# Optimization experiments

Measured on AMD Instinct MI355X. Metric: run time of the kernel, lower is better.

The kernel has to match this reference:

```python
import jax, jax.numpy as jnp
import numpy as np

N = 262144   # active voxels
C = 128      # channels (in == out)
B, Z, Y, X = 2, 41, 512, 512
EPS = 1e-3   # BN eps from norm_cfg


def _build_neighbors():
    """Build submanifold rulebook-style neighbor tables along z, y, x axes.
    Each table is [N, 3] (offsets -1, 0, +1); missing neighbor -> sentinel N
    (points at a zero-padded feature row)."""
    rng = np.random.default_rng(0)
    total = B * Z * Y * X
    lin = np.sort(rng.choice(total, size=N, replace=False)).astype(np.int64)
    lookup = np.full(total, -1, dtype=np.int64)
    lookup[lin] = np.arange(N)
    r = lin % (Z * Y * X)
    z = r // (Y * X)
    r2 = r % (Y * X)
    y = r2 // X
    x = r2 % X

    def nbrs(axis_vals, axis_size, stride):
        cols = []
        for off in (-1, 0, 1):
            v = axis_vals + off
            valid = (v >= 0) & (v < axis_size)
            nlin = np.clip(lin + off * stride, 0, total - 1)
            idx = np.where(valid, lookup[nlin], -1)
            idx = np.where(idx < 0, N, idx)
            cols.append(idx)
        return np.stack(cols, axis=1).astype(np.int32)

    return nbrs(z, Z, Y * X), nbrs(y, Y, X), nbrs(x, X, 1)


def setup_inputs() -> dict:
    key = jax.random.key(0)
    ks = jax.random.split(key, 8)
    nbr_z, nbr_y, nbr_x = _build_neighbors()
    scale = 1.0 / np.sqrt(3 * C)
    inp = {
        "features": jax.random.normal(ks[0], (N, C), dtype=jnp.float32),
        "W1": jax.random.normal(ks[1], (3, C, C), dtype=jnp.float32) * scale,  # conv3x1x1
        "W2": jax.random.normal(ks[2], (3, C, C), dtype=jnp.float32) * scale,  # conv1x3x1
        "W3": jax.random.normal(ks[3], (3, C, C), dtype=jnp.float32) * scale,  # conv1x1x3
        "g0": jax.random.normal(ks[4], (C,), dtype=jnp.float32) * 0.1 + 1.0,
        "b0": jnp.zeros((C,), dtype=jnp.float32),
        "m0": jax.random.normal(ks[5], (C,), dtype=jnp.float32) * 0.1,
        "v0": jax.random.uniform(ks[5], (C,), minval=0.5, maxval=1.5, dtype=jnp.float32),
        "g2": jax.random.normal(ks[6], (C,), dtype=jnp.float32) * 0.1 + 1.0,
        "b2": jnp.zeros((C,), dtype=jnp.float32),
        "m2": jax.random.normal(ks[6], (C,), dtype=jnp.float32) * 0.1,
        "v2": jax.random.uniform(ks[6], (C,), minval=0.5, maxval=1.5, dtype=jnp.float32),
        "g3": jax.random.normal(ks[7], (C,), dtype=jnp.float32) * 0.1 + 1.0,
        "b3": jnp.zeros((C,), dtype=jnp.float32),
        "m3": jax.random.normal(ks[7], (C,), dtype=jnp.float32) * 0.1,
        "v3": jax.random.uniform(ks[7], (C,), minval=0.5, maxval=1.5, dtype=jnp.float32),
        "nbr_z": jnp.asarray(nbr_z),
        "nbr_y": jnp.asarray(nbr_y),
        "nbr_x": jnp.asarray(nbr_x),
    }
    return inp


def _subm_conv(feats, nbr, W):
    # submanifold gather-matmul: out[n] = sum_k W[k] @ feats[nbr[n,k]] (sentinel -> 0)
    feats_pad = jnp.concatenate([feats, jnp.zeros((1, feats.shape[1]), feats.dtype)], axis=0)
    gathered = feats_pad[nbr]  # [N, 3, C]
    return jnp.einsum('nkc,kcd->nd', gathered, W)


def _bn(x, g, b, m, v):
    return (x - m) * (g * jax.lax.rsqrt(v + EPS)) + b


def reference(features, W1, W2, W3, g0, b0, m0, v0, g2, b2, m2, v2,
              g3, b3, m3, v3, nbr_z, nbr_y, nbr_x):
    # Branch 1: conv3x1x1 -> bn0 -> sigmoid, then (source bug) bn0_2 -> sigmoid applied again
    s = jax.nn.sigmoid(_bn(_subm_conv(features, nbr_z, W1), g0, b0, m0, v0))
    s = jax.nn.sigmoid(_bn(s, g2, b2, m2, v2))
    # Branch 2: conv1x3x1, added raw (its BN/act were mistakenly applied to branch 1)
    s2 = _subm_conv(features, nbr_y, W2)
    # Branch 3: conv1x1x3 -> bn0_3 -> sigmoid
    s3 = jax.nn.sigmoid(_bn(_subm_conv(features, nbr_x, W3), g3, b3, m3, v3))
    return (s + s2 + s3) * features
```

## Files before the change

### kernel.cpp

```cpp
#include <hip/hip_runtime.h>
#include <hip/hip_bf16.h>
#include <stdint.h>
#include <stddef.h>

#define NVOX 262144
#define CCH 128
#define BN_EPS 1e-3f

typedef __attribute__((ext_vector_type(8))) short bfrag;
typedef __attribute__((ext_vector_type(4))) float f4;

#define AS1 __attribute__((address_space(1)))
#define AS3 __attribute__((address_space(3)))

__device__ __forceinline__ unsigned short f2bf(float f) {
  union { float f; unsigned u; } v; v.f = f;
  unsigned r = v.u + 0x7fffu + ((v.u >> 16) & 1u);
  return (unsigned short)(r >> 16);
}

__device__ __forceinline__ bfrag pack8(f4 x, f4 y) {
  bfrag r;
  r[0] = (short)f2bf(x[0]); r[1] = (short)f2bf(x[1]);
  r[2] = (short)f2bf(x[2]); r[3] = (short)f2bf(x[3]);
  r[4] = (short)f2bf(y[0]); r[5] = (short)f2bf(y[1]);
  r[6] = (short)f2bf(y[2]); r[7] = (short)f2bf(y[3]);
  return r;
}

__device__ __forceinline__ float sigmoidf_(float x) {
  const float e = __builtin_amdgcn_exp2f(x * -1.44269504f);
  return __builtin_amdgcn_rcpf(1.f + e);
}

__device__ __forceinline__ float bf2f(unsigned short h) {
  union { unsigned u; float f; } v; v.u = ((unsigned)h) << 16; return v.f;
}

__global__ void prep_wfrag(const float* __restrict__ W1, const float* __restrict__ W2,
                           const float* __restrict__ W3, unsigned short* __restrict__ wf) {
  const int frag = blockIdx.x;
  const int tile = frag & 7;
  const int kc   = (frag >> 3) & 3;
  const int tap  = (frag >> 5) % 3;
  const int conv = frag / 96;
  const float* W = (conv == 0) ? W1 : ((conv == 1) ? W2 : W3);
  const int l   = threadIdx.x;
  const int col = tile * 16 + (l & 15);
  const int k0  = kc * 32 + (l >> 4) * 8;
  bfrag o;
#pragma unroll
  for (int e = 0; e < 8; ++e)
    o[e] = (short)f2bf(W[(size_t)(tap * CCH + k0 + e) * CCH + col]);
  *reinterpret_cast<bfrag*>(wf + (size_t)frag * 512 + l * 8) = o;
}

__global__ void prep_bn(const float* g0, const float* b0, const float* m0, const float* v0,
                        const float* g2, const float* b2, const float* m2, const float* v2,
                        const float* g3, const float* b3, const float* m3, const float* v3,
                        float* __restrict__ bn) {
  const int c = threadIdx.x;
  const float s0 = g0[c] * rsqrtf(v0[c] + BN_EPS);
  const float s2 = g2[c] * rsqrtf(v2[c] + BN_EPS);
  const float s3 = g3[c] * rsqrtf(v3[c] + BN_EPS);
  bn[0 * CCH + c] = s0; bn[1 * CCH + c] = b0[c] - m0[c] * s0;
  bn[2 * CCH + c] = s2; bn[3 * CCH + c] = b2[c] - m2[c] * s2;
  bn[4 * CCH + c] = s3; bn[5 * CCH + c] = b3[c] - m3[c] * s3;
}

__global__ void prep_bf16(const float* __restrict__ feats, unsigned short* __restrict__ fbf) {
  const size_t base = ((size_t)blockIdx.x * 256 + threadIdx.x) * 8;
  const f4 x = *reinterpret_cast<const f4*>(feats + base);
  const f4 y = *reinterpret_cast<const f4*>(feats + base + 4);
  *reinterpret_cast<bfrag*>(fbf + base) = pack8(x, y);
  if (blockIdx.x == 0 && threadIdx.x < 16) {
    bfrag z = {0, 0, 0, 0, 0, 0, 0, 0};
    *reinterpret_cast<bfrag*>(fbf + (size_t)NVOX * CCH + threadIdx.x * 8) = z;
  }
}

__global__ __launch_bounds__(512, 3)
void recon_v20(const unsigned short* __restrict__ fbf,
               const unsigned short* __restrict__ wfrag,
               const float* __restrict__ bn,
               const int* __restrict__ nbrz, const int* __restrict__ nbrx,
               const int* __restrict__ nbry,
               float* __restrict__ out) {
  __shared__ unsigned short Bb[24576];

  const int tid  = threadIdx.x;
  const int lane = tid & 63;
  const int w    = tid >> 6;
  const int l15  = lane & 15;
  const int lhi  = lane >> 4;
  const int cb   = blockIdx.x & 1;
  const int row0 = (blockIdx.x >> 1) * 128;
  const int wrow = row0 + w * 16;

  auto fillconv = [&](int RB) {
#pragma unroll
    for (int i = 0; i < 6; ++i) {
      const int L    = w * 6 + i;
      const int slot = L >> 4;
      const int sub  = L & 15;
      const int g    = ((RB + slot) * 4 + (sub >> 2)) * 8 + cb * 4 + (sub & 3);
      __builtin_amdgcn_global_load_lds(
          (const AS1 void*)(wfrag + (size_t)g * 512 + lane * 8),
          (AS3 void*)((char*)Bb + L * 1024), 16, 0, 0);
    }
  };

  fillconv(0);
  const int row = wrow + l15;
  const int rg  = row * 3;
  const int izp = nbrz[rg + 0], izn = nbrz[rg + 2];
  const int ixp = nbrx[rg + 0], ixn = nbrx[rg + 2];
  const int iyp = nbry[rg + 0], iyn = nbry[rg + 2];

  const bool azp = __any(izp != NVOX), azn = __any(izn != NVOX);
  const bool axp = __any(ixp != NVOX), axn = __any(ixn != NVOX);
  const bool ayp = __any(iyp != NVOX), ayn = __any(iyn != NVOX);

  bfrag aF[4];
  bfrag aS[4];

#define LOADF(DST, IDX) {                                                     \
    const char* p = (const char*)fbf + ((size_t)(unsigned)(IDX) << 8) + (lhi << 4); \
    DST[0] = *reinterpret_cast<const bfrag*>(p);                              \
    DST[1] = *reinterpret_cast<const bfrag*>(p + 64);                         \
    DST[2] = *reinterpret_cast<const bfrag*>(p + 128);                        \
    DST[3] = *reinterpret_cast<const bfrag*>(p + 192);                        \
  }

#define TAP(SLOT, AFR, ACCS) {                                                \
    const char* bs = (const char*)Bb + (SLOT) * 16384 + lane * 16;            \
    _Pragma("unroll")                                                         \
    for (int kc = 0; kc < 4; ++kc) {                                          \
      _Pragma("unroll")                                                       \
      for (int ct = 0; ct < 4; ++ct) {                                        \
        const bfrag b = *reinterpret_cast<const bfrag*>(                      \
            bs + (kc * 4 + ct) * 1024);                                       \
        ACCS[ct] = __builtin_amdgcn_mfma_f32_16x16x32_bf16(                   \
            AFR[kc], b, ACCS[ct], 0, 0, 0);                                   \
      } } }

#define CONVBODY(VP, VN, IN, ACCS)                                            \
  {                                                                           \
    TAP(1, aS, ACCS)                                                          \
    if (VP) {                                                                 \
      TAP(0, aF, ACCS)                                                        \
      if (VN) { LOADF(aF, IN)  TAP(2, aF, ACCS) }                             \
    } else if (VN) {                                                          \
      TAP(2, aF, ACCS)                                                        \
    }                                                                         \
  }

  LOADF(aS, row)
  if (azp)      LOADF(aF, izp)
  else if (azn) LOADF(aF, izn)

  __syncthreads();

  f4 acc[4], run[4];
#pragma unroll
  for (int ct = 0; ct < 4; ++ct) {
    acc[ct] = f4{0.f, 0.f, 0.f, 0.f};
    run[ct] = f4{0.f, 0.f, 0.f, 0.f};
  }

  CONVBODY(azp, azn, izn, acc)
  __syncthreads();
  fillconv(6);
  if (axp)      LOADF(aF, ixp)
  else if (axn) LOADF(aF, ixn)
#pragma unroll
  for (int ct = 0; ct < 4; ++ct) {
    const int col = cb * 64 + ct * 16 + l15;
    const float sc0 = bn[0 * CCH + col], sh0 = bn[1 * CCH + col];
    const float sc2 = bn[2 * CCH + col], sh2 = bn[3 * CCH + col];
#pragma unroll
    for (int j = 0; j < 4; ++j) {
      const float u = sigmoidf_(sc0 * acc[ct][j] + sh0);
      run[ct][j] = sigmoidf_(sc2 * u + sh2);
    }
    acc[ct] = f4{0.f, 0.f, 0.f, 0.f};
  }
  __syncthreads();

  CONVBODY(axp, axn, ixn, acc)
  __syncthreads();
  fillconv(3);
  if (ayp)      LOADF(aF, iyp)
  else if (ayn) LOADF(aF, iyn)
#pragma unroll
  for (int ct = 0; ct < 4; ++ct) {
    const int col = cb * 64 + ct * 16 + l15;
    const float sc3 = bn[4 * CCH + col], sh3 = bn[5 * CCH + col];
#pragma unroll
    for (int j = 0; j < 4; ++j)
      run[ct][j] += sigmoidf_(sc3 * acc[ct][j] + sh3);
  }
  __syncthreads();

  CONVBODY(ayp, ayn, iyn, run)

#undef CONVBODY
#undef TAP
#undef LOADF

#pragma unroll
  for (int ct = 0; ct < 4; ++ct) {
    const int col = cb * 64 + ct * 16 + l15;
#pragma unroll
    for (int j = 0; j < 4; ++j) {
      const int r = wrow + (lhi << 2) + j;
      const size_t o = ((size_t)r << 7) + col;
      out[o] = run[ct][j] * bf2f(fbf[o]);
    }
  }
}

__global__ void recon_naive(const float* __restrict__ feats,
    const float* __restrict__ W1, const float* __restrict__ W2, const float* __restrict__ W3,
    const int* __restrict__ nbrz, const int* __restrict__ nbry, const int* __restrict__ nbrx,
    const float* g0, const float* b0, const float* m0, const float* v0,
    const float* g2, const float* b2, const float* m2, const float* v2,
    const float* g3, const float* b3, const float* m3, const float* v3,
    float* __restrict__ out) {
  __shared__ float rows[3][CCH];
  const int n = blockIdx.x;
  const int d = threadIdx.x;
  float res[3];
#pragma unroll
  for (int conv = 0; conv < 3; ++conv) {
    const int* nbr  = (conv == 0) ? nbrz : ((conv == 1) ? nbry : nbrx);
    const float* W  = (conv == 0) ? W1 : ((conv == 1) ? W2 : W3);
#pragma unroll
    for (int tap = 0; tap < 3; ++tap) {
      const int idx = nbr[n * 3 + tap];
      rows[tap][d] = ((unsigned)idx < (unsigned)NVOX) ? feats[((size_t)idx << 7) + d] : 0.f;
    }
    __syncthreads();
    const float* rflat = &rows[0][0];
    float s = 0.f;
    for (int k = 0; k < 3 * CCH; ++k) s += rflat[k] * W[(size_t)k * CCH + d];
    res[conv] = s;
    __syncthreads();
  }
  const float sc0 = g0[d] * rsqrtf(v0[d] + BN_EPS), sh0 = b0[d] - m0[d] * sc0;
  const float sc2 = g2[d] * rsqrtf(v2[d] + BN_EPS), sh2 = b2[d] - m2[d] * sc2;
  const float sc3 = g3[d] * rsqrtf(v3[d] + BN_EPS), sh3 = b3[d] - m3[d] * sc3;
  float u = 1.f / (1.f + __expf(-(sc0 * res[0] + sh0)));
  u = 1.f / (1.f + __expf(-(sc2 * u + sh2)));
  const float s3v = 1.f / (1.f + __expf(-(sc3 * res[2] + sh3)));
  out[((size_t)n << 7) + d] = (u + res[1] + s3v) * feats[((size_t)n << 7) + d];
}

extern "C" void kernel_launch(void* const* d_in, const int* in_sizes, int n_in,
                              void* d_out, int out_size, void* d_ws, size_t ws_size,
                              hipStream_t stream) {
  const float* feats = (const float*)d_in[0];
  const float* W1 = (const float*)d_in[1];
  const float* W2 = (const float*)d_in[2];
  const float* W3 = (const float*)d_in[3];
  const float* g0 = (const float*)d_in[4];
  const float* b0 = (const float*)d_in[5];
  const float* m0 = (const float*)d_in[6];
  const float* v0 = (const float*)d_in[7];
  const float* g2 = (const float*)d_in[8];
  const float* b2 = (const float*)d_in[9];
  const float* m2 = (const float*)d_in[10];
  const float* v2 = (const float*)d_in[11];
  const float* g3 = (const float*)d_in[12];
  const float* b3 = (const float*)d_in[13];
  const float* m3 = (const float*)d_in[14];
  const float* v3 = (const float*)d_in[15];
  const int* nz = (const int*)d_in[16];
  const int* ny = (const int*)d_in[17];
  const int* nx = (const int*)d_in[18];
  float* out = (float*)d_out;

  const size_t wf_bytes = 288u * 1024u;
  const size_t bn_bytes = 4096u;
  const size_t fb_bytes = ((size_t)NVOX + 1) * CCH * sizeof(short);
  if (ws_size >= wf_bytes + bn_bytes + fb_bytes) {
    unsigned short* wf  = (unsigned short*)d_ws;
    float*          bnt = (float*)((char*)d_ws + wf_bytes);
    unsigned short* fbf = (unsigned short*)((char*)d_ws + wf_bytes + bn_bytes);
    hipLaunchKernelGGL(prep_wfrag, dim3(288), dim3(64), 0, stream, W1, W2, W3, wf);
    hipLaunchKernelGGL(prep_bn, dim3(1), dim3(CCH), 0, stream,
                       g0, b0, m0, v0, g2, b2, m2, v2, g3, b3, m3, v3, bnt);
    hipLaunchKernelGGL(prep_bf16, dim3((NVOX * CCH) / (256 * 8)), dim3(256), 0, stream,
                       feats, fbf);
    hipLaunchKernelGGL(recon_v20, dim3((NVOX / 128) * 2), dim3(512), 0, stream,
                       fbf, wf, bnt, nz, nx, ny, out);
  } else {
    hipLaunchKernelGGL(recon_naive, dim3(NVOX), dim3(CCH), 0, stream,
                       feats, W1, W2, W3, nz, ny, nx,
                       g0, b0, m0, v0, g2, b2, m2, v2, g3, b3, m3, v3, out);
  }
}
```

Measured before the change: 139.2 us.

## Replace syncthreads with partial vmcnt waits and sched barriers to overlap loads

Swaps each __syncthreads for a raw s_barrier preceded by an explicit partial s_waitcnt vmcnt. This waits only for the LDS weight fills, so the in-flight feature gathers can stay outstanding across the barrier. It also hoists the BN parameter loads ahead of the weight fill, adds sched_barrier fences to pin instruction order, and lowers the launch-bounds occupancy hint from 3 to 2 blocks per CU. The hand-counted vmcnt values depend on the exact number of outstanding loads. If the compiler emits a different number, the code can race or read stale data, and the lower occupancy hint may reduce latency hiding.

After: 172.8 us. 1.24x slower.

```diff
diff --git a/kernel.cpp b/kernel.cpp
--- a/kernel.cpp
+++ b/kernel.cpp
@@ -79,8 +79,8 @@
   }
 }
 
-__global__ __launch_bounds__(512, 3)
-void recon_v20(const unsigned short* __restrict__ fbf,
+__global__ __launch_bounds__(512, 2)
+void recon_v22(const unsigned short* __restrict__ fbf,
                const unsigned short* __restrict__ wfrag,
                const float* __restrict__ bn,
                const int* __restrict__ nbrz, const int* __restrict__ nbrx,
@@ -109,20 +109,6 @@
           (AS3 void*)((char*)Bb + L * 1024), 16, 0, 0);
     }
   };
-
-  fillconv(0);
-  const int row = wrow + l15;
-  const int rg  = row * 3;
-  const int izp = nbrz[rg + 0], izn = nbrz[rg + 2];
-  const int ixp = nbrx[rg + 0], ixn = nbrx[rg + 2];
-  const int iyp = nbry[rg + 0], iyn = nbry[rg + 2];
-
-  const bool azp = __any(izp != NVOX), azn = __any(izn != NVOX);
-  const bool axp = __any(ixp != NVOX), axn = __any(ixn != NVOX);
-  const bool ayp = __any(iyp != NVOX), ayn = __any(iyn != NVOX);
-
-  bfrag aF[4];
-  bfrag aS[4];
 
 #define LOADF(DST, IDX) {                                                     \
     const char* p = (const char*)fbf + ((size_t)(unsigned)(IDX) << 8) + (lhi << 4); \
@@ -155,11 +141,32 @@
     }                                                                         \
   }
 
+#define SB() __builtin_amdgcn_sched_barrier(0)
+
+  const int row = wrow + l15;
+  const int rg  = row * 3;
+  const int izp = nbrz[rg + 0], izn = nbrz[rg + 2];
+  const int ixp = nbrx[rg + 0], ixn = nbrx[rg + 2];
+  const int iyp = nbry[rg + 0], iyn = nbry[rg + 2];
+  SB();
+  fillconv(0);
+  SB();
+
+  bfrag aF[4];
+  bfrag aS[4];
+
   LOADF(aS, row)
+  const bool azp = __any(izp != NVOX), azn = __any(izn != NVOX);
+  const bool axp = __any(ixp != NVOX), axn = __any(ixn != NVOX);
+  const bool ayp = __any(iyp != NVOX), ayn = __any(iyn != NVOX);
   if (azp)      LOADF(aF, izp)
   else if (azn) LOADF(aF, izn)
-
-  __syncthreads();
+  SB();
+  if (azp || azn) { asm volatile("s_waitcnt vmcnt(8)" ::: "memory"); }
+  else            { asm volatile("s_waitcnt vmcnt(4)" ::: "memory"); }
+  SB();
+  __builtin_amdgcn_s_barrier();
+  SB();
 
   f4 acc[4], run[4];
 #pragma unroll
@@ -169,41 +176,71 @@
   }
 
   CONVBODY(azp, azn, izn, acc)
-  __syncthreads();
+  SB();
+  __builtin_amdgcn_s_barrier();
+  SB();
+
+  float s0v[4], h0v[4], s2v[4], h2v[4];
+#pragma unroll
+  for (int ct = 0; ct < 4; ++ct) {
+    const int col = cb * 64 + ct * 16 + l15;
+    s0v[ct] = bn[0 * CCH + col]; h0v[ct] = bn[1 * CCH + col];
+    s2v[ct] = bn[2 * CCH + col]; h2v[ct] = bn[3 * CCH + col];
+  }
+  SB();
   fillconv(6);
+  SB();
   if (axp)      LOADF(aF, ixp)
   else if (axn) LOADF(aF, ixn)
-#pragma unroll
-  for (int ct = 0; ct < 4; ++ct) {
-    const int col = cb * 64 + ct * 16 + l15;
-    const float sc0 = bn[0 * CCH + col], sh0 = bn[1 * CCH + col];
-    const float sc2 = bn[2 * CCH + col], sh2 = bn[3 * CCH + col];
+  SB();
+#pragma unroll
+  for (int ct = 0; ct < 4; ++ct) {
 #pragma unroll
     for (int j = 0; j < 4; ++j) {
-      const float u = sigmoidf_(sc0 * acc[ct][j] + sh0);
-      run[ct][j] = sigmoidf_(sc2 * u + sh2);
+      const float u = sigmoidf_(s0v[ct] * acc[ct][j] + h0v[ct]);
+      run[ct][j] = sigmoidf_(s2v[ct] * u + h2v[ct]);
     }
     acc[ct] = f4{0.f, 0.f, 0.f, 0.f};
   }
-  __syncthreads();
+  SB();
+  if (axp || axn) { asm volatile("s_waitcnt vmcnt(4)" ::: "memory"); }
+  else            { asm volatile("s_waitcnt vmcnt(0)" ::: "memory"); }
+  SB();
+  __builtin_amdgcn_s_barrier();
+  SB();
 
   CONVBODY(axp, axn, ixn, acc)
-  __syncthreads();
+  SB();
+  __builtin_amdgcn_s_barrier();
+  SB();
+
+  float s3v[4], h3v[4];
+#pragma unroll
+  for (int ct = 0; ct < 4; ++ct) {
+    const int col = cb * 64 + ct * 16 + l15;
+    s3v[ct] = bn[4 * CCH + col]; h3v[ct] = bn[5 * CCH + col];
+  }
+  SB();
   fillconv(3);
+  SB();
   if (ayp)      LOADF(aF, iyp)
   else if (ayn) LOADF(aF, iyn)
-#pragma unroll
-  for (int ct = 0; ct < 4; ++ct) {
-    const int col = cb * 64 + ct * 16 + l15;
-    const float sc3 = bn[4 * CCH + col], sh3 = bn[5 * CCH + col];
+  SB();
+#pragma unroll
+  for (int ct = 0; ct < 4; ++ct)
 #pragma unroll
     for (int j = 0; j < 4; ++j)
-      run[ct][j] += sigmoidf_(sc3 * acc[ct][j] + sh3);
-  }
-  __syncthreads();
+      run[ct][j] += sigmoidf_(s3v[ct] * acc[ct][j] + h3v[ct]);
+  SB();
+  if (ayp || ayn) { asm volatile("s_waitcnt vmcnt(4)" ::: "memory"); }
+  else            { asm volatile("s_waitcnt vmcnt(0)" ::: "memory"); }
+  SB();
+  __builtin_amdgcn_s_barrier();
+  SB();
 
   CONVBODY(ayp, ayn, iyn, run)
 
+#undef SB
 #undef CONVBODY
 #undef TAP
 #undef LOADF
@@ -292,7 +329,7 @@
                        g0, b0, m0, v0, g2, b2, m2, v2, g3, b3, m3, v3, bnt);
     hipLaunchKernelGGL(prep_bf16, dim3((NVOX * CCH) / (256 * 8)), dim3(256), 0, stream,
                        feats, fbf);
-    hipLaunchKernelGGL(recon_v20, dim3((NVOX / 128) * 2), dim3(512), 0, stream,
+    hipLaunchKernelGGL(recon_v22, dim3((NVOX / 128) * 2), dim3(512), 0, stream,
                        fbf, wf, bnt, nz, nx, ny, out);
   } else {
     hipLaunchKernelGGL(recon_naive, dim3(NVOX), dim3(CCH), 0, stream,
```
